# Kernel optimization log

Measured on AMD Instinct MI355X. Metric: run time of the kernel, lower is better.

The kernel has to match this reference:

```python
import jax, jax.numpy as jnp
import numpy as np

DIM = 2048
N_HEADS = 32
N_KV = 8
HEAD_DIM = DIM // N_HEADS  # 64
N_REP = N_HEADS // N_KV    # 4
HALF = HEAD_DIM // 2
B = 2
T = 2048
THETA = 10000.0


def _rope(x, cos, sin):
    # x: [B,H,T,hd]; cos/sin: [T,HALF]. Pairs are interleaved (..., half, 2),
    # matching torch.view_as_complex on a (..., -1, 2) reshape.
    xr = x.reshape(x.shape[:-1] + (HALF, 2))
    x0, x1 = xr[..., 0], xr[..., 1]
    o0 = x0 * cos - x1 * sin
    o1 = x0 * sin + x1 * cos
    return jnp.stack([o0, o1], axis=-1).reshape(x.shape)


def setup_inputs() -> dict:
    key = jax.random.key(0)
    ks = jax.random.split(key, 6)
    x = jax.random.normal(ks[0], (B, T, DIM), dtype=jnp.float32)
    scale = 0.02
    wq = jax.random.normal(ks[1], (N_HEADS * HEAD_DIM, DIM), dtype=jnp.float32) * scale
    wk = jax.random.normal(ks[2], (N_KV * HEAD_DIM, DIM), dtype=jnp.float32) * scale
    wv = jax.random.normal(ks[3], (N_KV * HEAD_DIM, DIM), dtype=jnp.float32) * scale
    wo = jax.random.normal(ks[4], (DIM, DIM), dtype=jnp.float32) * scale
    # causal mask [1,1,T,T]
    mask = jnp.tril(jnp.ones((T, T), dtype=jnp.int32))[None, None]
    # RoPE tables (precompute_freqs_cis with theta=10000, scaling_factor=1.0)
    freqs = 1.0 / THETA ** (jnp.arange(HALF, dtype=jnp.float32) / HALF)
    angles = jnp.arange(2 * T, dtype=jnp.float32)[:, None] * freqs[None, :]
    return {"x": x, "mask": mask, "wq": wq, "wk": wk, "wv": wv, "wo": wo,
            "cos": jnp.cos(angles), "sin": jnp.sin(angles)}


def reference(x, mask, wq, wk, wv, wo, cos, sin):
    Bx, Tx, C = x.shape
    q = (x @ wq.T).reshape(Bx, Tx, N_HEADS, HEAD_DIM).transpose(0, 2, 1, 3)
    k = (x @ wk.T).reshape(Bx, Tx, N_KV, HEAD_DIM).transpose(0, 2, 1, 3)
    v = (x @ wv.T).reshape(Bx, Tx, N_KV, HEAD_DIM).transpose(0, 2, 1, 3)
    q = _rope(q, cos[:Tx], sin[:Tx])
    k = _rope(k, cos[:Tx], sin[:Tx])
    # GQA: head h attends to kv head h // N_REP (repeat_interleave semantics)
    qg = q.reshape(Bx, N_KV, N_REP, Tx, HEAD_DIM)
    att = jnp.einsum('bgrtd,bgsd->bgrts', qg, k) * (HEAD_DIM ** -0.5)
    m = mask[0, 0, :Tx, :Tx]  # broadcast over b,g,r
    att = jnp.where(m == 0, -jnp.inf, att)
    att = jax.nn.softmax(att, axis=-1)
    og = jnp.einsum('bgrts,bgsd->bgrtd', att, v)
    out = og.reshape(Bx, N_HEADS, Tx, HEAD_DIM).transpose(0, 2, 1, 3).reshape(Bx, Tx, C)
    return out @ wo.T
```

## Files before the change

### kernel.cpp

```cpp
#include <hip/hip_runtime.h>
#include <hip/hip_bf16.h>

typedef unsigned short u16;
typedef __attribute__((ext_vector_type(8))) short s16x8;
typedef __attribute__((ext_vector_type(4))) float f32x4;
typedef __attribute__((ext_vector_type(16))) float f32x16;
typedef __attribute__((ext_vector_type(4))) float f32x4v;
typedef __attribute__((ext_vector_type(4))) u16 u16x4;

#define DIM 2048
#define NH 32
#define NKV 8
#define HD 64
#define TT 2048
#define BB 2
#define MT (BB * TT)

__device__ __forceinline__ u16 f2bf(float f) {
    union { float f; unsigned u; } v; v.f = f;
    unsigned r = v.u + 0x7FFFu + ((v.u >> 16) & 1u);
    return (u16)(r >> 16);
}
__device__ __forceinline__ float bf2f(u16 h) {
    union { unsigned u; float f; } v; v.u = ((unsigned)h) << 16;
    return v.f;
}
__device__ __forceinline__ u16 cvtbf(float f) {
    __hip_bfloat16 hb = __float2bfloat16(f);
    return *reinterpret_cast<u16*>(&hb);
}
__device__ __forceinline__ void plane32swap(unsigned& a, unsigned& b) {
#if defined(__has_builtin)
#if __has_builtin(__builtin_amdgcn_permlane32_swap)
    auto t = __builtin_amdgcn_permlane32_swap((int)a, (int)b, false, false);
    a = (unsigned)t[0]; b = (unsigned)t[1];
#else
    asm volatile("v_permlane32_swap_b32 %0, %1" : "+v"(a), "+v"(b));
#endif
#else
    asm volatile("v_permlane32_swap_b32 %0, %1" : "+v"(a), "+v"(b));
#endif
}

__global__ void k_convert_all(const float* __restrict__ x, const float* __restrict__ wq,
                              const float* __restrict__ wk, const float* __restrict__ wv,
                              const float* __restrict__ wo,
                              u16* __restrict__ xb, u16* __restrict__ wqkv, u16* __restrict__ wob) {
    long i = (long)(blockIdx.x * 256 + threadIdx.x) * 4;
    const float* src; u16* dst; long o = i;
    if (o < 8388608L)            { src = x;  dst = xb; }
    else if ((o -= 8388608L) < 4194304L) { src = wq; dst = wqkv; }
    else if ((o -= 4194304L) < 1048576L) { src = wk; dst = wqkv + 4194304L; }
    else if ((o -= 1048576L) < 1048576L) { src = wv; dst = wqkv + 5242880L; }
    else { o -= 1048576L;          src = wo; dst = wob; }
    f32x4v f = *(const f32x4v*)(src + o);
    u16x4 out;
    #pragma unroll
    for (int e = 0; e < 4; ++e) out[e] = f2bf(f[e]);
    *(u16x4*)(dst + o) = out;
}

template<int BNF, bool OUTF32>
__global__ __launch_bounds__(512, 2) void k_gemm256(const u16* __restrict__ A, const u16* __restrict__ B,
                                                    void* __restrict__ C, int M, int N, int K) {
    constexpr int BN = 64 * BNF;
    constexpr int BH = 2048 * BNF;
    __shared__ u16 LDS[32768 + 4 * BH];
    const int nTn = N / BN;
    const int nwg = gridDim.x;
    const int wg = (blockIdx.x & 7) * (nwg >> 3) + (blockIdx.x >> 3);
    const int tm = wg / nTn, tn = wg % nTn;
    const int tid = threadIdx.x, wid = tid >> 6, lane = tid & 63;
    const int wr = wid >> 2, wc = wid & 3;
    const u16* Ab = A + (size_t)tm * 256 * K;
    const u16* Bb = B + (size_t)tn * BN * K;

    f32x4 acc[8][BNF] = {};
    s16x8 af[4], bfr[BNF];

    auto STAGE_A = [&](int buf, int kk, int kt) {
        u16* base = LDS + (buf * 2 + kk) * 8192;
        const u16* g = Ab + kt * 64 + kk * 32;
        #pragma unroll
        for (int i = 0; i < 2; ++i) {
            const int s = i * 512 + tid;
            const int row = s >> 2;
            const int cl = (s & 3) ^ ((row >> 1) & 3);
            __builtin_amdgcn_global_load_lds(
                (const __attribute__((address_space(1))) void*)(g + (size_t)row * K + cl * 8),
                (__attribute__((address_space(3))) void*)(base + (i * 512 + wid * 64) * 8), 16, 0, 0);
        }
    };
    auto STAGE_B = [&](int buf, int kk, int kt) {
        u16* base = LDS + 32768 + (buf * 2 + kk) * BH;
        const u16* g = Bb + kt * 64 + kk * 32;
        auto one = [&](int ch) {
            const int row = ch * 16 + (lane >> 2);
            const int cl = (lane & 3) ^ ((row >> 1) & 3);
            __builtin_amdgcn_global_load_lds(
                (const __attribute__((address_space(1))) void*)(g + (size_t)row * K + cl * 8),
                (__attribute__((address_space(3))) void*)(base + ch * 512), 16, 0, 0);
        };
        if constexpr (BNF == 4) { one(wid); one(8 + wid); }
        else if constexpr (BNF == 3) { one(wid); one(8 + (wid & 3)); }
        else { one(wid); }
    };
    auto LDA = [&](int buf, int kk, int mh) {
        const u16* base = LDS + (buf * 2 + kk) * 8192;
        #pragma unroll
        for (int m2 = 0; m2 < 4; ++m2) {
            const int row = wr * 128 + (mh * 4 + m2) * 16 + (lane & 15);
            const int cl = (lane >> 4) ^ ((row >> 1) & 3);
            af[m2] = *(const s16x8*)(base + row * 32 + cl * 8);
        }
    };
    auto LDB = [&](int buf, int kk) {
        const u16* base = LDS + 32768 + (buf * 2 + kk) * BH;
        #pragma unroll
        for (int n = 0; n < BNF; ++n) {
            const int row = wc * (16 * BNF) + n * 16 + (lane & 15);
            const int cl = (lane >> 4) ^ ((row >> 1) & 3);
            bfr[n] = *(const s16x8*)(base + row * 32 + cl * 8);
        }
    };
    auto MFMA16 = [&](int mh) {
        asm volatile("s_waitcnt lgkmcnt(0)" ::: "memory");
        __builtin_amdgcn_sched_barrier(0);
        __builtin_amdgcn_s_setprio(1);
        #pragma unroll
        for (int m2 = 0; m2 < 4; ++m2)
            #pragma unroll
            for (int n = 0; n < BNF; ++n)
                acc[mh * 4 + m2][n] =
                    __builtin_amdgcn_mfma_f32_16x16x32_bf16(af[m2], bfr[n], acc[mh * 4 + m2][n], 0, 0, 0);
        __builtin_amdgcn_s_setprio(0);
    };

    #define VMID() do { if constexpr (BNF == 2) asm volatile("s_waitcnt vmcnt(6)" ::: "memory"); \
                        else                    asm volatile("s_waitcnt vmcnt(8)" ::: "memory"); } while (0)
    #define VONE() do { if constexpr (BNF == 2) asm volatile("s_waitcnt vmcnt(3)" ::: "memory"); \
                        else                    asm volatile("s_waitcnt vmcnt(4)" ::: "memory"); } while (0)

    STAGE_A(0, 0, 0); STAGE_B(0, 0, 0);
    STAGE_A(0, 1, 0); STAGE_B(0, 1, 0);
    STAGE_A(1, 0, 1); STAGE_B(1, 0, 1);
    VMID();
    __builtin_amdgcn_s_barrier();

    const int NI = K >> 7;
    for (int it = 0; it < NI; ++it) {
        const bool last = (it == NI - 1);
        const int t1 = 2 * it + 1;
        LDA(0, 0, 0); LDB(0, 0);
        STAGE_A(1, 1, t1);
        __builtin_amdgcn_s_barrier();
        MFMA16(0);
        __builtin_amdgcn_s_barrier();

        LDA(0, 0, 1);
        STAGE_B(1, 1, t1);
        __builtin_amdgcn_s_barrier();
        MFMA16(1);
        VMID();
        __builtin_amdgcn_s_barrier();

        LDA(0, 1, 0); LDB(0, 1);
        if (!last) STAGE_A(0, 0, t1 + 1);
        __builtin_amdgcn_s_barrier();
        MFMA16(0);
        __builtin_amdgcn_s_barrier();

        LDA(0, 1, 1);
        if (!last) STAGE_B(0, 0, t1 + 1);
        __builtin_amdgcn_s_barrier();
        MFMA16(1);
        if (!last) VMID(); else VONE();
        __builtin_amdgcn_s_barrier();

        LDA(1, 0, 0); LDB(1, 0);
        if (!last) STAGE_A(0, 1, t1 + 1);
        __builtin_amdgcn_s_barrier();
        MFMA16(0);
        __builtin_amdgcn_s_barrier();

        LDA(1, 0, 1);
        if (!last) STAGE_B(0, 1, t1 + 1);
        __builtin_amdgcn_s_barrier();
        MFMA16(1);
        if (!last) VMID(); else asm volatile("s_waitcnt vmcnt(0)" ::: "memory");
        __builtin_amdgcn_s_barrier();

        LDA(1, 1, 0); LDB(1, 1);
        if (!last) STAGE_A(1, 0, t1 + 2);
        __builtin_amdgcn_s_barrier();
        MFMA16(0);
        __builtin_amdgcn_s_barrier();

        LDA(1, 1, 1);
        if (!last) STAGE_B(1, 0, t1 + 2);
        __builtin_amdgcn_s_barrier();
        MFMA16(1);
        if (!last) VMID();
        __builtin_amdgcn_s_barrier();
    }
    #undef VMID
    #undef VONE

    #pragma unroll
    for (int mf = 0; mf < 8; ++mf)
        #pragma unroll
        for (int n = 0; n < BNF; ++n)
            #pragma unroll
            for (int r = 0; r < 4; ++r) {
                const int row = tm * 256 + wr * 128 + mf * 16 + (lane >> 4) * 4 + r;
                const int col = tn * BN + wc * (16 * BNF) + n * 16 + (lane & 15);
                if (OUTF32) ((float*)C)[(size_t)row * N + col] = acc[mf][n][r];
                else        ((u16*)C)[(size_t)row * N + col] = f2bf(acc[mf][n][r]);
            }
}

__global__ void k_rope(const u16* __restrict__ qkv, const float* __restrict__ ct, const float* __restrict__ st,
                       u16* __restrict__ qo, u16* __restrict__ ko, u16* __restrict__ vo) {
    const int idx = blockIdx.x * 256 + threadIdx.x;
    const int c = idx % 384;
    const int bt = idx / 384;
    const int b = bt / TT, t = bt % TT;
    const s16x8 v = *(const s16x8*)(qkv + (size_t)bt * 3072 + c * 8);
    if (c < 320) {
        const bool isq = c < 256;
        const int base = isq ? c : c - 256;
        const int hh = base >> 3;
        const int di0 = (base & 7) * 4;
        const f32x4v cc = *(const f32x4v*)(ct + t * 32 + di0);
        const f32x4v ss = *(const f32x4v*)(st + t * 32 + di0);
        const float QS = isq ? 0.18033688f : 1.0f;
        s16x8 o;
        #pragma unroll
        for (int p = 0; p < 4; ++p) {
            const float x0 = bf2f((u16)v[2 * p]), x1 = bf2f((u16)v[2 * p + 1]);
            o[2 * p]     = (short)cvtbf((x0 * cc[p] - x1 * ss[p]) * QS);
            o[2 * p + 1] = (short)cvtbf((x0 * ss[p] + x1 * cc[p]) * QS);
        }
        u16* dst = isq ? (qo + ((size_t)(b * NH + hh) * TT + t) * HD + 2 * di0)
                       : (ko + ((size_t)(b * NKV + hh) * TT + t) * HD + 2 * di0);
        *(s16x8*)dst = o;
    } else {
        const int base = c - 320;
        const int hh = base >> 3;
        const int d0 = (base & 7) * 8;
        *(s16x8*)(vo + ((size_t)(b * NKV + hh) * TT + t) * HD + d0) = v;
    }
}

__global__ __launch_bounds__(256) void k_vtrans(const u16* __restrict__ vp, u16* __restrict__ vt) {
    __shared__ u16 tile[64][66];
    const int bg = blockIdx.x >> 5;
    const int t0 = (blockIdx.x & 31) * 64;
    const int tid = threadIdx.x;
    #pragma unroll
    for (int c = 0; c < 2; ++c) {
        const int idx = c * 256 + tid;
        const int tl = idx >> 3, dc = idx & 7;
        s16x8 v = *(const s16x8*)(vp + ((size_t)bg * TT + t0 + tl) * HD + dc * 8);
        *(s16x8*)(&tile[tl][dc * 8]) = v;
    }
    __syncthreads();
    #pragma unroll
    for (int c = 0; c < 2; ++c) {
        const int idx = c * 256 + tid;
        const int d = idx >> 3, tc = idx & 7;
        s16x8 v;
        #pragma unroll
        for (int e = 0; e < 8; ++e) v[e] = (short)tile[tc * 8 + e][d];
        *(s16x8*)(vt + ((size_t)bg * HD + d) * TT + t0 + tc * 8) = v;
    }
}

__global__ __launch_bounds__(256) void k_attn(const u16* __restrict__ Q, const u16* __restrict__ K,
                                              const u16* __restrict__ Vtg, u16* __restrict__ O) {
    const int bid = blockIdx.x;
    const int qt = 15 - (bid >> 6);
    const int bh = bid & 63;
    const int h = bh & 31;
    const int b = bh >> 5;
    const int g = h >> 2;
    __shared__ u16 Ks[3][4096];
    __shared__ u16 Vs[3][4096];
    const int tid = threadIdx.x, wave = tid >> 6, lane = tid & 63;
    const int c = lane & 31, hi = lane >> 5;
    const u16* Qg = Q + ((size_t)(b * NH + h) * TT + qt * 128) * HD;
    const u16* Kg = K + (size_t)(b * NKV + g) * TT * HD;
    const u16* Vg = Vtg + (size_t)(b * NKV + g) * HD * TT;

    s16x8 qa[4];
    #pragma unroll
    for (int kb = 0; kb < 4; ++kb)
        qa[kb] = *(const s16x8*)(Qg + (size_t)(wave * 32 + c) * HD + kb * 16 + hi * 8);

    const int klo = (lane & 7) * HD + (lane >> 3) * 8;
    const int vlo = (lane & 7) * TT + (lane >> 3) * 8;
    auto stage = [&](int jj, int bi) {
        u16* Kb = Ks[bi];
        u16* Vb = Vs[bi];
        #pragma unroll
        for (int u2 = 0; u2 < 2; ++u2) {
            const int u = wave * 2 + u2;
            __builtin_amdgcn_global_load_lds(
                (const __attribute__((address_space(1))) void*)(Kg + (size_t)jj * 4096 + u * 512 + klo),
                (__attribute__((address_space(3))) void*)(Kb + u * 512), 16, 0, 0);
            __builtin_amdgcn_global_load_lds(
                (const __attribute__((address_space(1))) void*)(Vg + (size_t)u * 8 * TT + jj * 64 + vlo),
                (__attribute__((address_space(3))) void*)(Vb + u * 512), 16, 0, 0);
        }
    };

    f32x16 acc0 = {}, acc1 = {};
    float l = 0.f;
    const int ntiles = 2 * qt + 2;
    const int rbk = (c >> 3) * 512 + (c & 7) * 8 + hi * 64;

    stage(0, 0);
    stage(1, 1);

    for (int j = 0; j < ntiles; ++j) {
        if (j < ntiles - 1) asm volatile("s_waitcnt vmcnt(4)" ::: "memory");
        else                asm volatile("s_waitcnt vmcnt(0)" ::: "memory");
        __builtin_amdgcn_s_barrier();
        if (j + 2 < ntiles) stage(j + 2, (j + 2) % 3);
        const int bi = j % 3;
        const u16* Kb = Ks[bi];
        const u16* Vb = Vs[bi];

        f32x16 s0 = {}, s1 = {};
        __builtin_amdgcn_s_setprio(1);
        #pragma unroll
        for (int kb = 0; kb < 4; ++kb) {
            const s16x8 kf0 = *(const s16x8*)(Kb + rbk + kb * 128);
            const s16x8 kf1 = *(const s16x8*)(Kb + rbk + kb * 128 + 2048);
            s0 = __builtin_amdgcn_mfma_f32_32x32x16_bf16(kf0, qa[kb], s0, 0, 0, 0);
            s1 = __builtin_amdgcn_mfma_f32_32x32x16_bf16(kf1, qa[kb], s1, 0, 0, 0);
        }
        __builtin_amdgcn_s_setprio(0);

        if (j >= ntiles - 2) {
            const int q_loc = wave * 32 + c;
            const int kb64 = (j - (ntiles - 2)) * 64;
            #pragma unroll
            for (int r = 0; r < 16; ++r) {
                const int crow = (r & 3) + 8 * (r >> 2) + 4 * hi;
                if (kb64 + crow > q_loc)      s0[r] = -1e30f;
                if (kb64 + 32 + crow > q_loc) s1[r] = -1e30f;
            }
        }
        #pragma unroll
        for (int r = 0; r < 16; ++r) {
            s0[r] = __builtin_amdgcn_exp2f(s0[r]); l += s0[r];
            s1[r] = __builtin_amdgcn_exp2f(s1[r]); l += s1[r];
        }

        unsigned W0[8], W1[8];
        #pragma unroll
        for (int m = 0; m < 8; ++m) {
            float a0f = s0[2 * m], a1f = s0[2 * m + 1];
            float b0f = s1[2 * m], b1f = s1[2 * m + 1];
            asm("v_cvt_pk_bf16_f32 %0, %1, %2" : "=v"(W0[m]) : "v"(a0f), "v"(a1f));
            asm("v_cvt_pk_bf16_f32 %0, %1, %2" : "=v"(W1[m]) : "v"(b0f), "v"(b1f));
        }
        s16x8 pa[4];
        #pragma unroll
        for (int ks = 0; ks < 4; ++ks) {
            const int base = 4 * (ks & 1);
            unsigned a0 = (ks < 2) ? W0[base + 0] : W1[base + 0];
            unsigned b0 = (ks < 2) ? W0[base + 2] : W1[base + 2];
            unsigned a1 = (ks < 2) ? W0[base + 1] : W1[base + 1];
            unsigned b1 = (ks < 2) ? W0[base + 3] : W1[base + 3];
            plane32swap(a0, b0);
            plane32swap(a1, b1);
            union { unsigned w[4]; s16x8 v; } u;
            u.w[0] = a0; u.w[1] = a1; u.w[2] = b0; u.w[3] = b1;
            pa[ks] = u.v;
        }

        __builtin_amdgcn_s_setprio(1);
        #pragma unroll
        for (int kb = 0; kb < 4; ++kb) {
            const s16x8 vb0 = *(const s16x8*)(Vb + rbk + kb * 128);
            const s16x8 vb1 = *(const s16x8*)(Vb + rbk + kb * 128 + 2048);
            acc0 = __builtin_amdgcn_mfma_f32_32x32x16_bf16(pa[kb], vb0, acc0, 0, 0, 0);
            acc1 = __builtin_amdgcn_mfma_f32_32x32x16_bf16(pa[kb], vb1, acc1, 0, 0, 0);
        }
        __builtin_amdgcn_s_setprio(0);
    }

    l += __shfl_xor(l, 32, 64);
    const float inv = 1.0f / l;
    #pragma unroll
    for (int r = 0; r < 16; ++r) {
        const int crow = (r & 3) + 8 * (r >> 2) + 4 * hi;
        const float li = __shfl(inv, crow, 64);
        const size_t row = (size_t)b * TT + qt * 128 + wave * 32 + crow;
        O[row * DIM + h * 64 + c]      = cvtbf(acc0[r] * li);
        O[row * DIM + h * 64 + 32 + c] = cvtbf(acc1[r] * li);
    }
}

extern "C" void kernel_launch(void* const* d_in, const int* in_sizes, int n_in,
                              void* d_out, int out_size, void* d_ws, size_t ws_size,
                              hipStream_t stream) {
    const float* x  = (const float*)d_in[0];
    const float* wq = (const float*)d_in[2];
    const float* wk = (const float*)d_in[3];
    const float* wv = (const float*)d_in[4];
    const float* wo = (const float*)d_in[5];
    const float* ct = (const float*)d_in[6];
    const float* st = (const float*)d_in[7];
    char* ws = (char*)d_ws;
    u16* xb   = (u16*)(ws);
    u16* wqkv = (u16*)(ws + 16777216);
    u16* wob  = (u16*)(ws + 29360128);
    u16* qkv  = (u16*)(ws + 37748736);
    u16* kr   = (u16*)(ws + 62914560);
    u16* vp   = (u16*)(ws + 67108864);
    u16* qr   = xb;
    u16* ao   = qkv;
    u16* vt   = wqkv;

    k_convert_all<<<18432, 256, 0, stream>>>(x, wq, wk, wv, wo, xb, wqkv, wob);

    k_gemm256<3, false><<<(MT / 256) * (3072 / 192), 512, 0, stream>>>(xb, wqkv, qkv, MT, 3072, DIM);
    k_rope<<<MT * 384 / 256, 256, 0, stream>>>(qkv, ct, st, qr, kr, vp);
    k_vtrans<<<BB * NKV * (TT / 64), 256, 0, stream>>>(vp, vt);
    k_attn<<<16 * 64, 256, 0, stream>>>(qr, kr, vt, ao);
    k_gemm256<2, true><<<(MT / 256) * (DIM / 128), 512, 0, stream>>>(ao, wob, d_out, MT, DIM, DIM);
}
```

Baseline: 176.1 us.

## Pair complementary causal query tiles per attention block to share K/V loads

```diff
diff --git a/kernel.cpp b/kernel.cpp
--- a/kernel.cpp
+++ b/kernel.cpp
@@ -279,7 +279,8 @@
 __global__ __launch_bounds__(256) void k_attn(const u16* __restrict__ Q, const u16* __restrict__ K,
                                               const u16* __restrict__ Vtg, u16* __restrict__ O) {
     const int bid = blockIdx.x;
-    const int qt = 15 - (bid >> 6);
+    const int qtA = bid >> 6;
+    const int qtB = 15 - qtA;
     const int bh = bid & 63;
     const int h = bh & 31;
     const int b = bh >> 5;
@@ -288,14 +289,17 @@
     __shared__ u16 Vs[3][4096];
     const int tid = threadIdx.x, wave = tid >> 6, lane = tid & 63;
     const int c = lane & 31, hi = lane >> 5;
-    const u16* Qg = Q + ((size_t)(b * NH + h) * TT + qt * 128) * HD;
     const u16* Kg = K + (size_t)(b * NKV + g) * TT * HD;
     const u16* Vg = Vtg + (size_t)(b * NKV + g) * HD * TT;
 
-    s16x8 qa[4];
+    const u16* QgA = Q + ((size_t)(b * NH + h) * TT + qtA * 128) * HD;
+    const u16* QgB = Q + ((size_t)(b * NH + h) * TT + qtB * 128) * HD;
+    s16x8 qaA[4], qaB[4];
     #pragma unroll
-    for (int kb = 0; kb < 4; ++kb)
-        qa[kb] = *(const s16x8*)(Qg + (size_t)(wave * 32 + c) * HD + kb * 16 + hi * 8);
+    for (int kb = 0; kb < 4; ++kb) {
+        qaA[kb] = *(const s16x8*)(QgA + (size_t)(wave * 32 + c) * HD + kb * 16 + hi * 8);
+        qaB[kb] = *(const s16x8*)(QgB + (size_t)(wave * 32 + c) * HD + kb * 16 + hi * 8);
+    }
 
     const int klo = (lane & 7) * HD + (lane >> 3) * 8;
     const int vlo = (lane & 7) * TT + (lane >> 3) * 8;
@@ -314,37 +318,10 @@
         }
     };
 
-    f32x16 acc0 = {}, acc1 = {};
-    float l = 0.f;
-    const int ntiles = 2 * qt + 2;
-    const int rbk = (c >> 3) * 512 + (c & 7) * 8 + hi * 64;
-
-    stage(0, 0);
-    stage(1, 1);
-
-    for (int j = 0; j < ntiles; ++j) {
-        if (j < ntiles - 1) asm volatile("s_waitcnt vmcnt(4)" ::: "memory");
-        else                asm volatile("s_waitcnt vmcnt(0)" ::: "memory");
-        __builtin_amdgcn_s_barrier();
-        if (j + 2 < ntiles) stage(j + 2, (j + 2) % 3);
-        const int bi = j % 3;
-        const u16* Kb = Ks[bi];
-        const u16* Vb = Vs[bi];
-
-        f32x16 s0 = {}, s1 = {};
-        __builtin_amdgcn_s_setprio(1);
-        #pragma unroll
-        for (int kb = 0; kb < 4; ++kb) {
-            const s16x8 kf0 = *(const s16x8*)(Kb + rbk + kb * 128);
-            const s16x8 kf1 = *(const s16x8*)(Kb + rbk + kb * 128 + 2048);
-            s0 = __builtin_amdgcn_mfma_f32_32x32x16_bf16(kf0, qa[kb], s0, 0, 0, 0);
-            s1 = __builtin_amdgcn_mfma_f32_32x32x16_bf16(kf1, qa[kb], s1, 0, 0, 0);
-        }
-        __builtin_amdgcn_s_setprio(0);
-
-        if (j >= ntiles - 2) {
-            const int q_loc = wave * 32 + c;
-            const int kb64 = (j - (ntiles - 2)) * 64;
+    const int q_loc = wave * 32 + c;
+    auto soft = [&](f32x16& s0, f32x16& s1, float& l, int dj, s16x8* pa) {
+        if (dj >= 0) {
+            const int kb64 = dj * 64;
             #pragma unroll
             for (int r = 0; r < 16; ++r) {
                 const int crow = (r & 3) + 8 * (r >> 2) + 4 * hi;
@@ -352,12 +329,13 @@
                 if (kb64 + 32 + crow > q_loc) s1[r] = -1e30f;
             }
         }
+        float t[4] = {0.f, 0.f, 0.f, 0.f};
         #pragma unroll
         for (int r = 0; r < 16; ++r) {
-            s0[r] = __builtin_amdgcn_exp2f(s0[r]); l += s0[r];
-            s1[r] = __builtin_amdgcn_exp2f(s1[r]); l += s1[r];
-        }
-
+            s0[r] = __builtin_amdgcn_exp2f(s0[r]); t[r & 3] += s0[r];
+            s1[r] = __builtin_amdgcn_exp2f(s1[r]); t[r & 3] += s1[r];
+        }
+        l += (t[0] + t[1]) + (t[2] + t[3]);
         unsigned W0[8], W1[8];
         #pragma unroll
         for (int m = 0; m < 8; ++m) {
@@ -366,7 +344,6 @@
             asm("v_cvt_pk_bf16_f32 %0, %1, %2" : "=v"(W0[m]) : "v"(a0f), "v"(a1f));
             asm("v_cvt_pk_bf16_f32 %0, %1, %2" : "=v"(W1[m]) : "v"(b0f), "v"(b1f));
         }
-        s16x8 pa[4];
         #pragma unroll
         for (int ks = 0; ks < 4; ++ks) {
             const int base = 4 * (ks & 1);
@@ -380,28 +357,89 @@
             u.w[0] = a0; u.w[1] = a1; u.w[2] = b0; u.w[3] = b1;
             pa[ks] = u.v;
         }
-
+    };
+
+    f32x16 aA0 = {}, aA1 = {}, aB0 = {}, aB1 = {};
+    float lA = 0.f, lB = 0.f;
+    const int rbk = (c >> 3) * 512 + (c & 7) * 8 + hi * 64;
+    const int jend = 2 * qtB + 1;
+
+    stage(0, 0);
+    stage(1, 1);
+
+    for (int j = 0; j <= jend; ++j) {
+        if (j < jend) asm volatile("s_waitcnt vmcnt(4)" ::: "memory");
+        else          asm volatile("s_waitcnt vmcnt(0)" ::: "memory");
+        __builtin_amdgcn_s_barrier();
+        if (j + 2 <= jend) stage(j + 2, (j + 2) % 3);
+        const u16* Kb = Ks[j % 3];
+        const u16* Vb = Vs[j % 3];
+        const bool Aact = (j <= 2 * qtA + 1);
+
+        f32x16 sA0 = {}, sA1 = {}, sB0 = {}, sB1 = {};
         __builtin_amdgcn_s_setprio(1);
-        #pragma unroll
-        for (int kb = 0; kb < 4; ++kb) {
-            const s16x8 vb0 = *(const s16x8*)(Vb + rbk + kb * 128);
-            const s16x8 vb1 = *(const s16x8*)(Vb + rbk + kb * 128 + 2048);
-            acc0 = __builtin_amdgcn_mfma_f32_32x32x16_bf16(pa[kb], vb0, acc0, 0, 0, 0);
-            acc1 = __builtin_amdgcn_mfma_f32_32x32x16_bf16(pa[kb], vb1, acc1, 0, 0, 0);
+        if (Aact) {
+            #pragma unroll
+            for (int kb = 0; kb < 4; ++kb) {
+                const s16x8 kf0 = *(const s16x8*)(Kb + rbk + kb * 128);
+                const s16x8 kf1 = *(const s16x8*)(Kb + rbk + kb * 128 + 2048);
+                sB0 = __builtin_amdgcn_mfma_f32_32x32x16_bf16(kf0, qaB[kb], sB0, 0, 0, 0);
+                sA0 = __builtin_amdgcn_mfma_f32_32x32x16_bf16(kf0, qaA[kb], sA0, 0, 0, 0);
+                sB1 = __builtin_amdgcn_mfma_f32_32x32x16_bf16(kf1, qaB[kb], sB1, 0, 0, 0);
+                sA1 = __builtin_amdgcn_mfma_f32_32x32x16_bf16(kf1, qaA[kb], sA1, 0, 0, 0);
+            }
+        } else {
+            #pragma unroll
+            for (int kb = 0; kb < 4; ++kb) {
+                const s16x8 kf0 = *(const s16x8*)(Kb + rbk + kb * 128);
+                const s16x8 kf1 = *(const s16x8*)(Kb + rbk + kb * 128 + 2048);
+                sB0 = __builtin_amdgcn_mfma_f32_32x32x16_bf16(kf0, qaB[kb], sB0, 0, 0, 0);
+                sB1 = __builtin_amdgcn_mfma_f32_32x32x16_bf16(kf1, qaB[kb], sB1, 0, 0, 0);
+            }
         }
         __builtin_amdgcn_s_setprio(0);
-    }
-
-    l += __shfl_xor(l, 32, 64);
-    const float inv = 1.0f / l;
-    #pragma unroll
-    for (int r = 0; r < 16; ++r) {
-        const int crow = (r & 3) + 8 * (r >> 2) + 4 * hi;
-        const float li = __shfl(inv, crow, 64);
-        const size_t row = (size_t)b * TT + qt * 128 + wave * 32 + crow;
-        O[row * DIM + h * 64 + c]      = cvtbf(acc0[r] * li);
-        O[row * DIM + h * 64 + 32 + c] = cvtbf(acc1[r] * li);
-    }
+
+        s16x8 paA[4], paB[4];
+        if (Aact) soft(sA0, sA1, lA, j - 2 * qtA, paA);
+        soft(sB0, sB1, lB, j - 2 * qtB, paB);
+
+        __builtin_amdgcn_s_setprio(1);
+        if (Aact) {
+            #pragma unroll
+            for (int kb = 0; kb < 4; ++kb) {
+                const s16x8 vb0 = *(const s16x8*)(Vb + rbk + kb * 128);
+                const s16x8 vb1 = *(const s16x8*)(Vb + rbk + kb * 128 + 2048);
+                aB0 = __builtin_amdgcn_mfma_f32_32x32x16_bf16(paB[kb], vb0, aB0, 0, 0, 0);
+                aA0 = __builtin_amdgcn_mfma_f32_32x32x16_bf16(paA[kb], vb0, aA0, 0, 0, 0);
+                aB1 = __builtin_amdgcn_mfma_f32_32x32x16_bf16(paB[kb], vb1, aB1, 0, 0, 0);
+                aA1 = __builtin_amdgcn_mfma_f32_32x32x16_bf16(paA[kb], vb1, aA1, 0, 0, 0);
+            }
+        } else {
+            #pragma unroll
+            for (int kb = 0; kb < 4; ++kb) {
+                const s16x8 vb0 = *(const s16x8*)(Vb + rbk + kb * 128);
+                const s16x8 vb1 = *(const s16x8*)(Vb + rbk + kb * 128 + 2048);
+                aB0 = __builtin_amdgcn_mfma_f32_32x32x16_bf16(paB[kb], vb0, aB0, 0, 0, 0);
+                aB1 = __builtin_amdgcn_mfma_f32_32x32x16_bf16(paB[kb], vb1, aB1, 0, 0, 0);
+            }
+        }
+        __builtin_amdgcn_s_setprio(0);
+    }
+
+    auto epi = [&](f32x16& a0, f32x16& a1, float l, int qt) {
+        l += __shfl_xor(l, 32, 64);
+        const float inv = 1.0f / l;
+        #pragma unroll
+        for (int r = 0; r < 16; ++r) {
+            const int crow = (r & 3) + 8 * (r >> 2) + 4 * hi;
+            const float li = __shfl(inv, crow, 64);
+            const size_t row = (size_t)b * TT + qt * 128 + wave * 32 + crow;
+            O[row * DIM + h * 64 + c]      = cvtbf(a0[r] * li);
+            O[row * DIM + h * 64 + 32 + c] = cvtbf(a1[r] * li);
+        }
+    };
+    epi(aA0, aA1, lA, qtA);
+    epi(aB0, aB1, lB, qtB);
 }
 
 extern "C" void kernel_launch(void* const* d_in, const int* in_sizes, int n_in,
@@ -430,6 +468,6 @@
     k_gemm256<3, false><<<(MT / 256) * (3072 / 192), 512, 0, stream>>>(xb, wqkv, qkv, MT, 3072, DIM);
     k_rope<<<MT * 384 / 256, 256, 0, stream>>>(qkv, ct, st, qr, kr, vp);
     k_vtrans<<<BB * NKV * (TT / 64), 256, 0, stream>>>(vp, vt);
-    k_attn<<<16 * 64, 256, 0, stream>>>(qr, kr, vt, ao);
+    k_attn<<<8 * 64, 256, 0, stream>>>(qr, kr, vt, ao);
     k_gemm256<2, true><<<(MT / 256) * (DIM / 128), 512, 0, stream>>>(ao, wob, d_out, MT, DIM, DIM);
 }
```

Result: slower. 224.4 us (+27.4%).
